# Performance work log

Hardware: AMD Instinct MI355X
Metric: run time of the kernel (lower is better)

## Reference

```python
import jax, jax.numpy as jnp
import numpy as np

P = 16          # patch size
NUM_HEADS = 8
WINDOW = 64     # window_size from SparseAttention(window_size=64)


def _layer_norm(x, w, b, eps=1e-5):
    mu = jnp.mean(x, axis=-1, keepdims=True)
    var = jnp.var(x, axis=-1, keepdims=True)
    return (x - mu) * jax.lax.rsqrt(var + eps) * w + b


def _sinusoidal_pe(num_patches, num_features, dtype):
    pos = jnp.arange(num_patches, dtype=jnp.float32)[:, None]            # [N,1]
    i = jnp.arange(0, num_features, 2, dtype=jnp.float32)                # [D/2]
    div = jnp.exp(-jnp.log(10000.0) * i / num_features)                  # [D/2]
    ang = pos * div                                                      # [N,D/2]
    pe = jnp.stack([jnp.sin(ang), jnp.cos(ang)], axis=-1).reshape(num_patches, num_features)
    return pe.astype(dtype)


def _ffn(x, w1, b1, w2, b2):
    # FeedForward: Linear -> GELU -> Linear (dropout inactive at eval)
    h = jax.nn.gelu(jnp.einsum('bnd,hd->bnh', x, w1) + b1)
    return jnp.einsum('bnh,dh->bnd', h, w2) + b2


def _windowed_attention(x, qkv_w, qkv_b, proj_w, proj_b):
    B, N, D = x.shape
    hd = D // NUM_HEADS
    qkv = jnp.einsum('bnd,ed->bne', x, qkv_w) + qkv_b                    # [B,N,3D]
    qkv = qkv.reshape(B, N, 3, NUM_HEADS, hd)
    q, k, v = qkv[:, :, 0], qkv[:, :, 1], qkv[:, :, 2]                   # [B,N,H,hd]
    nw = N // WINDOW
    # partition sequence into non-overlapping windows of 64 tokens
    q = q.reshape(B, nw, WINDOW, NUM_HEADS, hd).transpose(0, 3, 1, 2, 4)  # [B,H,nw,W,hd]
    k = k.reshape(B, nw, WINDOW, NUM_HEADS, hd).transpose(0, 3, 1, 2, 4)
    v = v.reshape(B, nw, WINDOW, NUM_HEADS, hd).transpose(0, 3, 1, 2, 4)
    scale = 1.0 / jnp.sqrt(jnp.asarray(hd, x.dtype))
    scores = jnp.einsum('bhwqd,bhwkd->bhwqk', q, k) * scale              # [B,H,nw,W,W]
    attn = jax.nn.softmax(scores, axis=-1)
    out = jnp.einsum('bhwqk,bhwkd->bhwqd', attn, v)                      # [B,H,nw,W,hd]
    out = out.transpose(0, 2, 3, 1, 4).reshape(B, N, D)
    return jnp.einsum('bnd,ed->bne', out, proj_w) + proj_b


def setup_inputs() -> dict:
    key = jax.random.key(0)
    ks = jax.random.split(key, 8)
    D, HF = 256, 1024
    s = lambda fan: 1.0 / np.sqrt(fan)
    return {
        'x': jax.random.normal(ks[0], (32, 3, 512, 512), jnp.float32),
        'conv_w': jax.random.normal(ks[1], (D, 3, P, P), jnp.float32) * s(3 * P * P),
        'conv_b': jnp.zeros((D,), jnp.float32),
        'ln_w': jnp.ones((D,), jnp.float32),
        'ln_b': jnp.zeros((D,), jnp.float32),
        'qkv_w': jax.random.normal(ks[2], (3 * D, D), jnp.float32) * s(D),
        'qkv_b': jnp.zeros((3 * D,), jnp.float32),
        'proj_w': jax.random.normal(ks[3], (D, D), jnp.float32) * s(D),
        'proj_b': jnp.zeros((D,), jnp.float32),
        'ff_w1': jax.random.normal(ks[4], (HF, D), jnp.float32) * s(D),
        'ff_b1': jnp.zeros((HF,), jnp.float32),
        'ff_w2': jax.random.normal(ks[5], (D, HF), jnp.float32) * s(HF),
        'ff_b2': jnp.zeros((D,), jnp.float32),
    }


def reference(x, conv_w, conv_b, ln_w, ln_b, qkv_w, qkv_b, proj_w, proj_b,
              ff_w1, ff_b1, ff_w2, ff_b2):
    B, C, H, W = x.shape
    D = conv_w.shape[0]
    # PatchEmbedding1: Conv2d(C, D, kernel=16, stride=16) == per-patch matmul, then LayerNorm
    nH, nW = H // P, W // P
    patches = x.reshape(B, C, nH, P, nW, P).transpose(0, 2, 4, 1, 3, 5).reshape(B, nH * nW, C * P * P)
    h = jnp.einsum('bnp,dp->bnd', patches, conv_w.reshape(D, -1)) + conv_b
    h = _layer_norm(h, ln_w, ln_b)
    # static sinusoidal position embedding
    h = h + _sinusoidal_pe(h.shape[1], D, h.dtype)
    # block 1: FFN -> sparse (windowed) attention -> residual
    identity = h
    h = _ffn(h, ff_w1, ff_b1, ff_w2, ff_b2)
    h = _windowed_attention(h, qkv_w, qkv_b, proj_w, proj_b)
    h = h + identity
    # block 2: shared FFN -> residual
    identity = h
    h = _ffn(h, ff_w1, ff_b1, ff_w2, ff_b2)
    return h + identity
```

## Files before the change

kernel.cpp:

```cpp
#include <hip/hip_runtime.h>
#include <math.h>


#define M_TOK 32768

typedef __attribute__((ext_vector_type(8))) short  short8;
typedef __attribute__((ext_vector_type(4))) float  f32x4;
typedef __attribute__((ext_vector_type(8))) unsigned short us8v;
typedef __attribute__((ext_vector_type(4))) unsigned short us4v;

__device__ __forceinline__ unsigned short f2b(float f) {
    union { float f; unsigned u; } c; c.f = f;
    unsigned r = c.u + 0x7fffu + ((c.u >> 16) & 1u);
    return (unsigned short)(r >> 16);
}
__device__ __forceinline__ float gelu_fast(float x) {
    const float c0 = 0.7978845608028654f;
    const float c1 = 0.044715f * 0.7978845608028654f;
    float z = x * (c0 + c1 * x * x);
    float e = __expf(-2.0f * z);
    return x * __builtin_amdgcn_rcpf(1.0f + e);
}
__device__ __forceinline__ void load_lds16(const unsigned short* g, void* lds) {
    __builtin_amdgcn_global_load_lds(
        (const __attribute__((address_space(1))) unsigned int*)g,
        (__attribute__((address_space(3))) unsigned int*)lds, 16, 0, 0);
}

__global__ __launch_bounds__(256) void cvt_f2b_kernel(
    const float* __restrict__ in, unsigned short* __restrict__ out, int n)
{
    int i = (blockIdx.x * 256 + threadIdx.x) * 4;
    if (i >= n) return;
    float4 v = *(const float4*)(in + i);
    us4v o;
    o[0] = f2b(v.x); o[1] = f2b(v.y); o[2] = f2b(v.z); o[3] = f2b(v.w);
    *(us4v*)(out + i) = o;
}

__global__ __launch_bounds__(256) void pe_init_kernel(float* __restrict__ pe)
{
    const int pos = blockIdx.x;
    const int d   = threadIdx.x;
    const int ieven = d & ~1;
    float div = expf(-9.210340371976184f * (float)ieven * (1.0f / 256.0f));
    float ang = (float)pos * div;
    pe[pos * 256 + d] = (d & 1) ? cosf(ang) : sinf(ang);
}

template<bool GELU, bool RES, bool WF32, bool WB16>
__global__ __launch_bounds__(256) void mfma_gemm_kernel(
    const unsigned short* __restrict__ A, const unsigned short* __restrict__ W,
    const float* __restrict__ bias, const float* __restrict__ res,
    float* __restrict__ outF, unsigned short* __restrict__ outB,
    int M, int N, int K)
{
    __shared__ unsigned short As[128 * 32];
    __shared__ unsigned short Ws[128 * 32];

    const int t    = threadIdx.x;
    const int m0   = blockIdx.x * 128;
    const int n0   = blockIdx.y * 128;
    const int wv   = t >> 6, lane = t & 63;
    const int wr   = (wv >> 1) * 64, wc = (wv & 1) * 64;
    const int l15  = lane & 15, quad = lane >> 4;

    f32x4 acc[4][4];
#pragma unroll
    for (int i = 0; i < 4; i++)
#pragma unroll
        for (int j = 0; j < 4; j++)
#pragma unroll
            for (int r = 0; r < 4; r++) acc[i][j][r] = 0.0f;

    const int srow = wv * 16 + (lane >> 2);
    const int skk  = (lane & 3) * 8;
    const unsigned short* gA0 = A + (size_t)(m0 + srow) * K + skk;
    const unsigned short* gA1 = gA0 + (size_t)64 * K;
    const unsigned short* gW0 = W + (size_t)(n0 + srow) * K + skk;
    const unsigned short* gW1 = gW0 + (size_t)64 * K;
    char* lA0 = (char*)As + wv * 1024;
    char* lA1 = lA0 + 4096;
    char* lW0 = (char*)Ws + wv * 1024;
    char* lW1 = lW0 + 4096;

    for (int k0 = 0; k0 < K; k0 += 32) {
        __syncthreads();
        load_lds16(gA0 + k0, lA0);
        load_lds16(gA1 + k0, lA1);
        load_lds16(gW0 + k0, lW0);
        load_lds16(gW1 + k0, lW1);
        __syncthreads();

        short8 af[4], wf[4];
#pragma unroll
        for (int i = 0; i < 4; i++)
            af[i] = *(const short8*)&As[(wr + i * 16 + l15) * 32 + quad * 8];
#pragma unroll
        for (int j = 0; j < 4; j++)
            wf[j] = *(const short8*)&Ws[(wc + j * 16 + l15) * 32 + quad * 8];
#pragma unroll
        for (int i = 0; i < 4; i++)
#pragma unroll
            for (int j = 0; j < 4; j++)
                acc[i][j] = __builtin_amdgcn_mfma_f32_16x16x32_bf16(
                    af[i], wf[j], acc[i][j], 0, 0, 0);
    }

#pragma unroll
    for (int i = 0; i < 4; i++) {
        const int gr = m0 + wr + i * 16 + quad * 4;
#pragma unroll
        for (int j = 0; j < 4; j++) {
            const int gc = n0 + wc + j * 16 + l15;
            const float bv = bias[gc];
#pragma unroll
            for (int r = 0; r < 4; r++) {
                float v = acc[i][j][r] + bv;
                if (GELU) v = gelu_fast(v);
                if (RES)  v += res[(size_t)(gr + r) * N + gc];
                if (WF32) outF[(size_t)(gr + r) * N + gc] = v;
                if (WB16) outB[(size_t)(gr + r) * N + gc] = f2b(v);
            }
        }
    }
}

__global__ __launch_bounds__(256) void patch_mfma_kernel(
    const unsigned short* __restrict__ xb, const unsigned short* __restrict__ W,
    const float* __restrict__ bias, float* __restrict__ outF)
{
    __shared__ unsigned short As[128 * 32];
    __shared__ unsigned short Ws[128 * 32];

    const int t    = threadIdx.x;
    const int m0   = blockIdx.x * 128;
    const int n0   = blockIdx.y * 128;
    const int wv   = t >> 6, lane = t & 63;
    const int wr   = (wv >> 1) * 64, wc = (wv & 1) * 64;
    const int l15  = lane & 15, quad = lane >> 4;

    f32x4 acc[4][4];
#pragma unroll
    for (int i = 0; i < 4; i++)
#pragma unroll
        for (int j = 0; j < 4; j++)
#pragma unroll
            for (int r = 0; r < 4; r++) acc[i][j][r] = 0.0f;

    const int srow = wv * 16 + (lane >> 2);
    const int skk  = (lane & 3) * 8;
    size_t xoff[2];
#pragma unroll
    for (int s = 0; s < 2; s++) {
        const int m  = m0 + s * 64 + srow;
        const int b  = m >> 10;
        const int idx = m & 1023;
        const int hh = idx >> 5, ww = idx & 31;
        xoff[s] = ((size_t)(b * 3) * 512 + (size_t)(hh * 16)) * 512 + ww * 16;
    }
    const unsigned short* gW0 = W + (size_t)(n0 + srow) * 768 + skk;
    const unsigned short* gW1 = gW0 + (size_t)64 * 768;
    char* lA0 = (char*)As + wv * 1024;
    char* lA1 = lA0 + 4096;
    char* lW0 = (char*)Ws + wv * 1024;
    char* lW1 = lW0 + 4096;

    for (int k0 = 0; k0 < 768; k0 += 32) {
        const int k  = k0 + skk;
        const int c  = k >> 8;
        const int ph = (k >> 4) & 15;
        const int pw = k & 15;
        const size_t koff = (size_t)c * 262144 + (size_t)ph * 512 + pw;
        __syncthreads();
        load_lds16(xb + xoff[0] + koff, lA0);
        load_lds16(xb + xoff[1] + koff, lA1);
        load_lds16(gW0 + k0, lW0);
        load_lds16(gW1 + k0, lW1);
        __syncthreads();

        short8 af[4], wf[4];
#pragma unroll
        for (int i = 0; i < 4; i++)
            af[i] = *(const short8*)&As[(wr + i * 16 + l15) * 32 + quad * 8];
#pragma unroll
        for (int j = 0; j < 4; j++)
            wf[j] = *(const short8*)&Ws[(wc + j * 16 + l15) * 32 + quad * 8];
#pragma unroll
        for (int i = 0; i < 4; i++)
#pragma unroll
            for (int j = 0; j < 4; j++)
                acc[i][j] = __builtin_amdgcn_mfma_f32_16x16x32_bf16(
                    af[i], wf[j], acc[i][j], 0, 0, 0);
    }

#pragma unroll
    for (int i = 0; i < 4; i++) {
        const int gr = m0 + wr + i * 16 + quad * 4;
#pragma unroll
        for (int j = 0; j < 4; j++) {
            const int gc = n0 + wc + j * 16 + l15;
            const float bv = bias[gc];
#pragma unroll
            for (int r = 0; r < 4; r++)
                outF[(size_t)(gr + r) * 256 + gc] = acc[i][j][r] + bv;
        }
    }
}

__global__ __launch_bounds__(256) void ln_pe_kernel(
    const float* __restrict__ in, const float* __restrict__ w,
    const float* __restrict__ b, const float* __restrict__ pe_t,
    float* __restrict__ outF, unsigned short* __restrict__ outB)
{
    const int m = blockIdx.x;
    const int d = threadIdx.x;
    float v = in[(size_t)m * 256 + d];

    float s = v, s2 = v * v;
#pragma unroll
    for (int off = 32; off > 0; off >>= 1) {
        s  += __shfl_down(s,  off, 64);
        s2 += __shfl_down(s2, off, 64);
    }
    __shared__ float ss[4], ss2[4], stats[2];
    const int lane = d & 63, wid = d >> 6;
    if (lane == 0) { ss[wid] = s; ss2[wid] = s2; }
    __syncthreads();
    if (d == 0) {
        float a  = ss[0] + ss[1] + ss[2] + ss[3];
        float a2 = ss2[0] + ss2[1] + ss2[2] + ss2[3];
        float mean = a * (1.0f / 256.0f);
        float var  = a2 * (1.0f / 256.0f) - mean * mean;
        stats[0] = mean;
        stats[1] = rsqrtf(var + 1e-5f);
    }
    __syncthreads();
    const float mean = stats[0], rstd = stats[1];

    const int pos = m & 1023;
    float pe = pe_t[pos * 256 + d];

    float o = (v - mean) * rstd * w[d] + b[d] + pe;
    outF[(size_t)m * 256 + d] = o;
    outB[(size_t)m * 256 + d] = f2b(o);
}

__global__ __launch_bounds__(256) void attn_mfma_kernel(
    const unsigned short* __restrict__ qkv, unsigned short* __restrict__ out)
{
    __shared__ unsigned short Ps[64 * 72];
    __shared__ unsigned short Vt[32 * 72];

    const int blk = blockIdx.x;
    const int h = blk & 7;
    const int w = (blk >> 3) & 15;
    const int b = blk >> 7;
    const int m_base = b * 1024 + w * 64;

    const int t = threadIdx.x;
    const int wv = t >> 6, lane = t & 63;
    const int l15 = lane & 15, quad = lane >> 4;

    {
        const int row = t >> 2;
        const int c0  = (t & 3) * 8;
        const unsigned short* src = qkv + (size_t)(m_base + row) * 768 + 512 + h * 32 + c0;
        us8v v = *(const us8v*)src;
#pragma unroll
        for (int j = 0; j < 8; j++) Vt[(c0 + j) * 72 + row] = v[j];
    }

    short8 aq = *(const short8*)(qkv + (size_t)(m_base + wv * 16 + l15) * 768 + h * 32 + quad * 8);
    f32x4 c[4];
#pragma unroll
    for (int j = 0; j < 4; j++) {
        short8 bk = *(const short8*)(qkv + (size_t)(m_base + j * 16 + l15) * 768 + 256 + h * 32 + quad * 8);
        f32x4 z = {0.0f, 0.0f, 0.0f, 0.0f};
        c[j] = __builtin_amdgcn_mfma_f32_16x16x32_bf16(aq, bk, z, 0, 0, 0);
    }

    const float scale = 0.17677669529663687f;
    float sm[4];
#pragma unroll
    for (int r = 0; r < 4; r++) {
        float m0 = -1e30f;
#pragma unroll
        for (int j = 0; j < 4; j++) { c[j][r] *= scale; m0 = fmaxf(m0, c[j][r]); }
#pragma unroll
        for (int d = 1; d < 16; d <<= 1) m0 = fmaxf(m0, __shfl_xor(m0, d, 64));
        float s0 = 0.0f;
#pragma unroll
        for (int j = 0; j < 4; j++) { float e = __expf(c[j][r] - m0); c[j][r] = e; s0 += e; }
#pragma unroll
        for (int d = 1; d < 16; d <<= 1) s0 += __shfl_xor(s0, d, 64);
        sm[r] = __builtin_amdgcn_rcpf(s0);
    }

#pragma unroll
    for (int r = 0; r < 4; r++) {
        const int prow = wv * 16 + quad * 4 + r;
#pragma unroll
        for (int j = 0; j < 4; j++)
            Ps[prow * 72 + j * 16 + l15] = f2b(c[j][r] * sm[r]);
    }
    __syncthreads();

    short8 ap0 = *(const short8*)&Ps[(wv * 16 + l15) * 72 + quad * 8];
    short8 ap1 = *(const short8*)&Ps[(wv * 16 + l15) * 72 + 32 + quad * 8];
    f32x4 o[2];
#pragma unroll
    for (int nt = 0; nt < 2; nt++) {
        short8 bv0 = *(const short8*)&Vt[(nt * 16 + l15) * 72 + quad * 8];
        short8 bv1 = *(const short8*)&Vt[(nt * 16 + l15) * 72 + 32 + quad * 8];
        f32x4 z = {0.0f, 0.0f, 0.0f, 0.0f};
        o[nt] = __builtin_amdgcn_mfma_f32_16x16x32_bf16(ap0, bv0, z, 0, 0, 0);
        o[nt] = __builtin_amdgcn_mfma_f32_16x16x32_bf16(ap1, bv1, o[nt], 0, 0, 0);
    }

#pragma unroll
    for (int nt = 0; nt < 2; nt++) {
#pragma unroll
        for (int r = 0; r < 4; r++) {
            const int row = m_base + wv * 16 + quad * 4 + r;
            out[(size_t)row * 256 + h * 32 + nt * 16 + l15] = f2b(o[nt][r]);
        }
    }
}

extern "C" void kernel_launch(void* const* d_in, const int* in_sizes, int n_in,
                              void* d_out, int out_size, void* d_ws, size_t ws_size,
                              hipStream_t stream)
{
    const float* x      = (const float*)d_in[0];
    const float* conv_w = (const float*)d_in[1];
    const float* conv_b = (const float*)d_in[2];
    const float* ln_w   = (const float*)d_in[3];
    const float* ln_b   = (const float*)d_in[4];
    const float* qkv_w  = (const float*)d_in[5];
    const float* qkv_b  = (const float*)d_in[6];
    const float* proj_w = (const float*)d_in[7];
    const float* proj_b = (const float*)d_in[8];
    const float* ff_w1  = (const float*)d_in[9];
    const float* ff_b1  = (const float*)d_in[10];
    const float* ff_w2  = (const float*)d_in[11];
    const float* ff_b2  = (const float*)d_in[12];
    float* out = (float*)d_out;

    char* ws = (char*)d_ws;
    unsigned short* xb    = (unsigned short*)(ws);
    unsigned short* hidb  = (unsigned short*)(ws);
    float*          h0    = (float*)(ws + 67108864);
    unsigned short* qkvb  = (unsigned short*)(ws + 67108864);
    float*          pe_t  = (float*)(ws + 100663296);
    float*          h1f   = (float*)(ws + 117440512);
    unsigned short* h1b   = (unsigned short*)(ws + 150994944);
    unsigned short* aob   = (unsigned short*)(ws + 150994944);
    unsigned short* f1b   = (unsigned short*)(ws + 167772160);
    unsigned short* h2b   = (unsigned short*)(ws + 167772160);
    unsigned short* wbase = (unsigned short*)(ws + 184549376);
    unsigned short* conv_wb = wbase;
    unsigned short* qkv_wb  = wbase + 196608;
    unsigned short* proj_wb = wbase + 393216;
    unsigned short* ff_w1b  = wbase + 458752;
    unsigned short* ff_w2b  = wbase + 720896;

    const int M = M_TOK;
    dim3 blk(256);

    cvt_f2b_kernel<<<dim3(25165824 / 1024), blk, 0, stream>>>(x, xb, 25165824);
    cvt_f2b_kernel<<<dim3(196608 / 1024), blk, 0, stream>>>(conv_w, conv_wb, 196608);
    cvt_f2b_kernel<<<dim3(196608 / 1024), blk, 0, stream>>>(qkv_w, qkv_wb, 196608);
    cvt_f2b_kernel<<<dim3(65536 / 1024), blk, 0, stream>>>(proj_w, proj_wb, 65536);
    cvt_f2b_kernel<<<dim3(262144 / 1024), blk, 0, stream>>>(ff_w1, ff_w1b, 262144);
    cvt_f2b_kernel<<<dim3(262144 / 1024), blk, 0, stream>>>(ff_w2, ff_w2b, 262144);
    pe_init_kernel<<<dim3(1024), blk, 0, stream>>>(pe_t);

    patch_mfma_kernel<<<dim3(M / 128, 2), blk, 0, stream>>>(xb, conv_wb, conv_b, h0);
    ln_pe_kernel<<<dim3(M), blk, 0, stream>>>(h0, ln_w, ln_b, pe_t, h1f, h1b);
    mfma_gemm_kernel<true, false, false, true><<<dim3(M / 128, 8), blk, 0, stream>>>(
        h1b, ff_w1b, ff_b1, nullptr, nullptr, hidb, M, 1024, 256);
    mfma_gemm_kernel<false, false, false, true><<<dim3(M / 128, 2), blk, 0, stream>>>(
        hidb, ff_w2b, ff_b2, nullptr, nullptr, f1b, M, 256, 1024);
    mfma_gemm_kernel<false, false, false, true><<<dim3(M / 128, 6), blk, 0, stream>>>(
        f1b, qkv_wb, qkv_b, nullptr, nullptr, qkvb, M, 768, 256);
    attn_mfma_kernel<<<dim3(4096), blk, 0, stream>>>(qkvb, aob);
    mfma_gemm_kernel<false, true, true, true><<<dim3(M / 128, 2), blk, 0, stream>>>(
        aob, proj_wb, proj_b, h1f, out, h2b, M, 256, 256);
    mfma_gemm_kernel<true, false, false, true><<<dim3(M / 128, 8), blk, 0, stream>>>(
        h2b, ff_w1b, ff_b1, nullptr, nullptr, hidb, M, 1024, 256);
    mfma_gemm_kernel<false, true, true, false><<<dim3(M / 128, 2), blk, 0, stream>>>(
        hidb, ff_w2b, ff_b2, out, out, nullptr, M, 256, 1024);
}
```

Baseline: 439.2 us.

## Double GEMM K-tile to 64 with XOR-swizzled LDS and fuse weight conversions

The MFMA GEMM and patch-embedding kernels now stage 64-wide K tiles instead of 32, which halves the number of barrier pairs per output tile. Global-to-LDS loads and fragment reads use an XOR swizzle on the column index so the wider rows avoid LDS bank conflicts. The five separate weight fp32-to-bf16 conversion launches are merged into one kernel that picks its source by block index, saving launch overhead. LDS use per block doubles, which may reduce occupancy.

```diff
diff --git a/kernel.cpp b/kernel.cpp
--- a/kernel.cpp
+++ b/kernel.cpp
@@ -38,6 +38,28 @@
     *(us4v*)(out + i) = o;
 }
 
+__global__ __launch_bounds__(256) void cvt_weights_kernel(
+    const float* __restrict__ s0, const float* __restrict__ s1,
+    const float* __restrict__ s2, const float* __restrict__ s3,
+    const float* __restrict__ s4,
+    unsigned short* __restrict__ d0, unsigned short* __restrict__ d1,
+    unsigned short* __restrict__ d2, unsigned short* __restrict__ d3,
+    unsigned short* __restrict__ d4)
+{
+    const int bid = blockIdx.x;
+    const float* src; unsigned short* dst; int off;
+    if      (bid < 192) { src = s0; dst = d0; off = bid; }
+    else if (bid < 384) { src = s1; dst = d1; off = bid - 192; }
+    else if (bid < 448) { src = s2; dst = d2; off = bid - 384; }
+    else if (bid < 704) { src = s3; dst = d3; off = bid - 448; }
+    else                { src = s4; dst = d4; off = bid - 704; }
+    const int i = off * 1024 + threadIdx.x * 4;
+    float4 v = *(const float4*)(src + i);
+    us4v o;
+    o[0] = f2b(v.x); o[1] = f2b(v.y); o[2] = f2b(v.z); o[3] = f2b(v.w);
+    *(us4v*)(dst + i) = o;
+}
+
 __global__ __launch_bounds__(256) void pe_init_kernel(float* __restrict__ pe)
 {
     const int pos = blockIdx.x;
@@ -55,8 +77,8 @@
     float* __restrict__ outF, unsigned short* __restrict__ outB,
     int M, int N, int K)
 {
-    __shared__ unsigned short As[128 * 32];
-    __shared__ unsigned short Ws[128 * 32];
+    __shared__ unsigned short As[128 * 64];
+    __shared__ unsigned short Ws[128 * 64];
 
     const int t    = threadIdx.x;
     const int m0   = blockIdx.x * 128;
@@ -73,38 +95,41 @@
 #pragma unroll
             for (int r = 0; r < 4; r++) acc[i][j][r] = 0.0f;
 
-    const int srow = wv * 16 + (lane >> 2);
-    const int skk  = (lane & 3) * 8;
-    const unsigned short* gA0 = A + (size_t)(m0 + srow) * K + skk;
-    const unsigned short* gA1 = gA0 + (size_t)64 * K;
-    const unsigned short* gW0 = W + (size_t)(n0 + srow) * K + skk;
-    const unsigned short* gW1 = gW0 + (size_t)64 * K;
-    char* lA0 = (char*)As + wv * 1024;
-    char* lA1 = lA0 + 4096;
-    char* lW0 = (char*)Ws + wv * 1024;
-    char* lW1 = lW0 + 4096;
-
-    for (int k0 = 0; k0 < K; k0 += 32) {
+    const int srow = wv * 8 + (lane >> 3);
+    const int skk  = (((lane & 7) ^ ((lane >> 3) & 7)) * 8);
+    const unsigned short* gA = A + (size_t)(m0 + srow) * K + skk;
+    const unsigned short* gW = W + (size_t)(n0 + srow) * K + skk;
+    char* lA = (char*)As + wv * 1024;
+    char* lW = (char*)Ws + wv * 1024;
+
+    const int cswz = (l15 & 7) * 8;
+
+    for (int k0 = 0; k0 < K; k0 += 64) {
         __syncthreads();
-        load_lds16(gA0 + k0, lA0);
-        load_lds16(gA1 + k0, lA1);
-        load_lds16(gW0 + k0, lW0);
-        load_lds16(gW1 + k0, lW1);
+#pragma unroll
+        for (int s = 0; s < 4; s++) {
+            load_lds16(gA + (size_t)(s * 32) * K + k0, lA + s * 4096);
+            load_lds16(gW + (size_t)(s * 32) * K + k0, lW + s * 4096);
+        }
         __syncthreads();
 
-        short8 af[4], wf[4];
-#pragma unroll
-        for (int i = 0; i < 4; i++)
-            af[i] = *(const short8*)&As[(wr + i * 16 + l15) * 32 + quad * 8];
-#pragma unroll
-        for (int j = 0; j < 4; j++)
-            wf[j] = *(const short8*)&Ws[(wc + j * 16 + l15) * 32 + quad * 8];
-#pragma unroll
-        for (int i = 0; i < 4; i++)
+#pragma unroll
+        for (int kh = 0; kh < 2; kh++) {
+            const int coff = (kh * 32 + quad * 8) ^ cswz;
+            short8 af[4], wf[4];
+#pragma unroll
+            for (int i = 0; i < 4; i++)
+                af[i] = *(const short8*)&As[(wr + i * 16 + l15) * 64 + coff];
 #pragma unroll
             for (int j = 0; j < 4; j++)
-                acc[i][j] = __builtin_amdgcn_mfma_f32_16x16x32_bf16(
-                    af[i], wf[j], acc[i][j], 0, 0, 0);
+                wf[j] = *(const short8*)&Ws[(wc + j * 16 + l15) * 64 + coff];
+#pragma unroll
+            for (int i = 0; i < 4; i++)
+#pragma unroll
+                for (int j = 0; j < 4; j++)
+                    acc[i][j] = __builtin_amdgcn_mfma_f32_16x16x32_bf16(
+                        af[i], wf[j], acc[i][j], 0, 0, 0);
+        }
     }
 
 #pragma unroll
@@ -130,8 +155,8 @@
     const unsigned short* __restrict__ xb, const unsigned short* __restrict__ W,
     const float* __restrict__ bias, float* __restrict__ outF)
 {
-    __shared__ unsigned short As[128 * 32];
-    __shared__ unsigned short Ws[128 * 32];
+    __shared__ unsigned short As[128 * 64];
+    __shared__ unsigned short Ws[128 * 64];
 
     const int t    = threadIdx.x;
     const int m0   = blockIdx.x * 128;
@@ -148,50 +173,54 @@
 #pragma unroll
             for (int r = 0; r < 4; r++) acc[i][j][r] = 0.0f;
 
-    const int srow = wv * 16 + (lane >> 2);
-    const int skk  = (lane & 3) * 8;
-    size_t xoff[2];
-#pragma unroll
-    for (int s = 0; s < 2; s++) {
-        const int m  = m0 + s * 64 + srow;
+    const int srow = wv * 8 + (lane >> 3);
+    const int skk  = (((lane & 7) ^ ((lane >> 3) & 7)) * 8);
+    size_t xoff[4];
+#pragma unroll
+    for (int s = 0; s < 4; s++) {
+        const int m  = m0 + s * 32 + srow;
         const int b  = m >> 10;
         const int idx = m & 1023;
         const int hh = idx >> 5, ww = idx & 31;
         xoff[s] = ((size_t)(b * 3) * 512 + (size_t)(hh * 16)) * 512 + ww * 16;
     }
-    const unsigned short* gW0 = W + (size_t)(n0 + srow) * 768 + skk;
-    const unsigned short* gW1 = gW0 + (size_t)64 * 768;
-    char* lA0 = (char*)As + wv * 1024;
-    char* lA1 = lA0 + 4096;
-    char* lW0 = (char*)Ws + wv * 1024;
-    char* lW1 = lW0 + 4096;
-
-    for (int k0 = 0; k0 < 768; k0 += 32) {
+    const unsigned short* gW = W + (size_t)(n0 + srow) * 768 + skk;
+    char* lA = (char*)As + wv * 1024;
+    char* lW = (char*)Ws + wv * 1024;
+
+    const int cswz = (l15 & 7) * 8;
+
+    for (int k0 = 0; k0 < 768; k0 += 64) {
         const int k  = k0 + skk;
         const int c  = k >> 8;
         const int ph = (k >> 4) & 15;
         const int pw = k & 15;
         const size_t koff = (size_t)c * 262144 + (size_t)ph * 512 + pw;
         __syncthreads();
-        load_lds16(xb + xoff[0] + koff, lA0);
-        load_lds16(xb + xoff[1] + koff, lA1);
-        load_lds16(gW0 + k0, lW0);
-        load_lds16(gW1 + k0, lW1);
+#pragma unroll
+        for (int s = 0; s < 4; s++) {
+            load_lds16(xb + xoff[s] + koff, lA + s * 4096);
+            load_lds16(gW + (size_t)(s * 32) * 768 + k0, lW + s * 4096);
+        }
         __syncthreads();
 
-        short8 af[4], wf[4];
-#pragma unroll
-        for (int i = 0; i < 4; i++)
-            af[i] = *(const short8*)&As[(wr + i * 16 + l15) * 32 + quad * 8];
-#pragma unroll
-        for (int j = 0; j < 4; j++)
-            wf[j] = *(const short8*)&Ws[(wc + j * 16 + l15) * 32 + quad * 8];
-#pragma unroll
-        for (int i = 0; i < 4; i++)
+#pragma unroll
+        for (int kh = 0; kh < 2; kh++) {
+            const int coff = (kh * 32 + quad * 8) ^ cswz;
+            short8 af[4], wf[4];
+#pragma unroll
+            for (int i = 0; i < 4; i++)
+                af[i] = *(const short8*)&As[(wr + i * 16 + l15) * 64 + coff];
 #pragma unroll
             for (int j = 0; j < 4; j++)
-                acc[i][j] = __builtin_amdgcn_mfma_f32_16x16x32_bf16(
-                    af[i], wf[j], acc[i][j], 0, 0, 0);
+                wf[j] = *(const short8*)&Ws[(wc + j * 16 + l15) * 64 + coff];
+#pragma unroll
+            for (int i = 0; i < 4; i++)
+#pragma unroll
+                for (int j = 0; j < 4; j++)
+                    acc[i][j] = __builtin_amdgcn_mfma_f32_16x16x32_bf16(
+                        af[i], wf[j], acc[i][j], 0, 0, 0);
+        }
     }
 
 #pragma unroll
@@ -369,11 +398,9 @@
     dim3 blk(256);
 
     cvt_f2b_kernel<<<dim3(25165824 / 1024), blk, 0, stream>>>(x, xb, 25165824);
-    cvt_f2b_kernel<<<dim3(196608 / 1024), blk, 0, stream>>>(conv_w, conv_wb, 196608);
-    cvt_f2b_kernel<<<dim3(196608 / 1024), blk, 0, stream>>>(qkv_w, qkv_wb, 196608);
-    cvt_f2b_kernel<<<dim3(65536 / 1024), blk, 0, stream>>>(proj_w, proj_wb, 65536);
-    cvt_f2b_kernel<<<dim3(262144 / 1024), blk, 0, stream>>>(ff_w1, ff_w1b, 262144);
-    cvt_f2b_kernel<<<dim3(262144 / 1024), blk, 0, stream>>>(ff_w2, ff_w2b, 262144);
+    cvt_weights_kernel<<<dim3(960), blk, 0, stream>>>(
+        conv_w, qkv_w, proj_w, ff_w1, ff_w2,
+        conv_wb, qkv_wb, proj_wb, ff_w1b, ff_w2b);
     pe_init_kernel<<<dim3(1024), blk, 0, stream>>>(pe_t);
 
     patch_mfma_kernel<<<dim3(M / 128, 2), blk, 0, stream>>>(xb, conv_wb, conv_b, h0);
```

After: 418.0 us. -4.8%, faster.
